# Optimization experiments

Hardware: AMD Instinct MI355X
Metric: run time of the kernel (lower is better)

## Reference

```python
import jax, jax.numpy as jnp
import numpy as np

N_ITEMS = 50000
HIDDEN = 128
M_NB = 16
HOP = 2
R_ITERS = 4
K_FACT = 10
B = 512
L = 50


def _normalize(x, eps=1e-12):
    n = jnp.linalg.norm(x, axis=-1, keepdims=True)
    return x / jnp.maximum(n, eps)


def _layernorm(x, g, b, eps=1e-5):
    mu = jnp.mean(x, axis=-1, keepdims=True)
    v = jnp.var(x, axis=-1, keepdims=True)
    return (x - mu) / jnp.sqrt(v + eps) * g + b


def _gru(x, h0, Wih, Whh, bih, bhh):
    # x: [B, L, H]; PyTorch GRU gate order: r, z, n
    def step(h, xt):
        gi = xt @ Wih.T + bih
        gh = h @ Whh.T + bhh
        ir, iz, inn = jnp.split(gi, 3, axis=-1)
        hr, hz, hn = jnp.split(gh, 3, axis=-1)
        r = jax.nn.sigmoid(ir + hr)
        zg = jax.nn.sigmoid(iz + hz)
        ng = jnp.tanh(inn + r * hn)
        h_new = (1.0 - zg) * ng + zg * h
        return h_new, h_new
    _, hs = jax.lax.scan(step, h0, jnp.swapaxes(x, 0, 1))
    return jnp.swapaxes(hs, 0, 1)


def _routing(x, x_nb):
    # NeighborRoutingAgg: x [n,d], x_nb [n,m] (1-based ids)
    xn = _normalize(x)
    z = xn[x_nb - 1]                      # [n, m, d] gather
    # iter 0: softmax(zeros) over neighbors is uniform -> mean
    u = jnp.mean(z, axis=1) + xn
    for _ in range(R_ITERS - 1):
        sq = jnp.sum(u * u, axis=1)
        u = (sq / (sq + 1.0))[:, None] * _normalize(u)   # squash
        p = jax.nn.softmax(jnp.einsum('nmd,nd->nm', z, u), axis=1)
        u = jnp.einsum('nmd,nm->nd', z, p) + xn
    return u


def setup_inputs() -> dict:
    key = jax.random.key(0)
    ks = jax.random.split(key, 16)
    H = HIDDEN
    s = 1.0 / np.sqrt(H)
    inp = {}
    inp['item_emb'] = jax.random.normal(ks[0], (N_ITEMS, H), dtype=jnp.float32) * 0.1
    inp['prob_emb'] = jax.random.normal(ks[1], (N_ITEMS, K_FACT), dtype=jnp.float32) * 0.1
    inp['W_cls'] = jax.random.normal(ks[2], (H, K_FACT), dtype=jnp.float32) * (1.0 / np.sqrt(K_FACT))
    inp['a1'] = jax.random.normal(ks[3], (1,), dtype=jnp.float32)
    inp['a2'] = jax.random.normal(ks[4], (1,), dtype=jnp.float32)
    inp['gru_Wih'] = jax.random.uniform(ks[5], (3 * H, H), minval=-s, maxval=s, dtype=jnp.float32)
    inp['gru_Whh'] = jax.random.uniform(ks[6], (3 * H, H), minval=-s, maxval=s, dtype=jnp.float32)
    inp['gru_bih'] = jax.random.uniform(ks[7], (3 * H,), minval=-s, maxval=s, dtype=jnp.float32)
    inp['gru_bhh'] = jax.random.uniform(ks[8], (3 * H,), minval=-s, maxval=s, dtype=jnp.float32)
    for nm in ['ln1', 'ln2', 'ln3', 'ln4']:
        inp[nm + '_g'] = jnp.ones((H,), dtype=jnp.float32)
        inp[nm + '_b'] = jnp.zeros((H,), dtype=jnp.float32)
    inp['mask_1'] = jnp.ones((B, L), dtype=jnp.float32)
    inp['mask_inf'] = jnp.zeros((B, L), dtype=jnp.float32)
    inp['inp_sess'] = jax.random.randint(ks[9], (B, L), 1, N_ITEMS)
    inp['lengths'] = jax.random.randint(ks[10], (B,), 1, L + 1)
    inp['adj_items'] = jax.random.randint(ks[11], (N_ITEMS, M_NB), 1, N_ITEMS)
    return inp


def reference(item_emb, prob_emb, W_cls, a1, a2, gru_Wih, gru_Whh, gru_bih, gru_bhh,
              ln1_g, ln1_b, ln2_g, ln2_b, ln3_g, ln3_b, ln4_g, ln4_b,
              mask_1, mask_inf, inp_sess, lengths, adj_items):
    H = HIDDEN
    x = item_emb[1:]                       # row 0 is padding
    x_nb = adj_items[1:]
    outs = [x]
    for i in range(HOP):
        outs.append(_routing(outs[i], x_nb))
    iv = outs[0]
    for o in outs[1:]:
        iv = iv + o
    iv = _layernorm(iv, ln1_g, ln1_b)      # [n_items-1, H]
    item_vectors = jnp.concatenate([jnp.zeros((1, H), dtype=iv.dtype), iv], axis=0)
    inp_emb = item_vectors[inp_sess]       # [B, L, H] (dropout = eval identity)
    bsz = inp_sess.shape[0]
    h0 = jnp.zeros((bsz, H), dtype=iv.dtype)
    Hs = _gru(inp_emb, h0, gru_Wih, gru_Whh, gru_bih, gru_bhh)
    Hs = _layernorm(Hs, ln2_g, ln2_b)
    ht = Hs[jnp.arange(bsz), lengths - 1]  # [B, H]
    inp_cls = prob_emb[inp_sess]           # [B, L, K]
    inp_cls_emb = _layernorm(inp_cls @ W_cls.T, ln3_g, ln3_b)
    Hc = _gru(inp_cls_emb, h0, gru_Wih, gru_Whh, gru_bih, gru_bhh)
    Hc = _layernorm(Hc, ln4_g, ln4_b)
    ht_cls = Hc[jnp.arange(bsz), lengths - 1]
    scores1 = ht @ iv.T                                           # [B, n_items-1]
    cls_tab = _layernorm(prob_emb[1:] @ W_cls.T, ln3_g, ln3_b)    # [n_items-1, H]
    scores2 = ht_cls @ cls_tab.T
    scores = jax.nn.sigmoid(a1) * scores1 + jax.nn.sigmoid(a2) * scores2
    return scores, scores1, scores2
```

## Files before the change

### kernel.cpp

```cpp
#include <hip/hip_runtime.h>
#include <hip/hip_bf16.h>

#define N_IT 49999
#define NI   50000
#define HD   128
#define MNB  16
#define BSZ  512
#define LSEQ 50
#define G3   384

typedef __attribute__((ext_vector_type(8))) short short8;
typedef __attribute__((ext_vector_type(4))) float f32x4;
typedef __attribute__((ext_vector_type(16))) float f32x16;

__device__ __forceinline__ float sigmf(float x) {
  return 1.f / (1.f + __expf(-x));
}
__device__ __forceinline__ float fast_sigm(float x) {
  return __fdividef(1.f, 1.f + __expf(-x));
}
__device__ __forceinline__ float fast_tanh(float x) {
  float e = __expf(-2.f * x);
  return (1.f - e) * __fdividef(1.f, 1.f + e);
}

__device__ __forceinline__ unsigned short f2bf(float f) {
  unsigned u = __float_as_uint(f);
  u += 0x7FFF + ((u >> 16) & 1);
  return (unsigned short)(u >> 16);
}

template <int CTRL>
__device__ __forceinline__ float dppadd(float v) {
  int s = __builtin_amdgcn_update_dpp(__float_as_int(v), __float_as_int(v),
                                      CTRL, 0xF, 0xF, false);
  return v + __int_as_float(s);
}
template <int MASK>
__device__ __forceinline__ float swzadd(float v) {
  return v + __int_as_float(__builtin_amdgcn_ds_swizzle(__float_as_int(v), MASK));
}
__device__ __forceinline__ float bp32add(float v) {
  int lane = threadIdx.x & 63;
  return v + __int_as_float(__builtin_amdgcn_ds_bpermute(((lane ^ 32) << 2),
                                                         __float_as_int(v)));
}

__device__ __forceinline__ float wsum(float v) {
  v = dppadd<0xB1>(v);
  v = dppadd<0x4E>(v);
  v = dppadd<0x141>(v);
  v = dppadd<0x140>(v);
  v = swzadd<0x401F>(v);
  v = bp32add(v);
  return v;
}

__global__ void norm_kernel(const float* __restrict__ x, float* __restrict__ o,
                            unsigned* __restrict__ ob, int n) {
  int w = threadIdx.x >> 6, l = threadIdx.x & 63;
  int r = blockIdx.x * 4 + w;
  if (r >= n) return;
  float2 xv = *(const float2*)(x + (size_t)r * HD + 2 * l);
  float sq = wsum(xv.x * xv.x + xv.y * xv.y);
  float inv = 1.f / fmaxf(sqrtf(sq), 1e-12f);
  float a = xv.x * inv, b = xv.y * inv;
  *(float2*)(o + (size_t)r * HD + 2 * l) = make_float2(a, b);
  ob[(size_t)r * 64 + l] = (unsigned)f2bf(a) | ((unsigned)f2bf(b) << 16);
}

__global__ __launch_bounds__(256) void routing1_kernel(
    const float* __restrict__ xn, const unsigned* __restrict__ xnb,
    const int* __restrict__ adj, float* __restrict__ out,
    float* __restrict__ onf, unsigned* __restrict__ onb) {
  __shared__ char zsh[4][4096];
  int tid = threadIdx.x;
  int w = tid >> 6, lane = tid & 63;
  int n = blockIdx.x * 4 + w;
  if (n >= N_IT) return;
  int m = lane & 15, quad = lane >> 4;
  const unsigned short* xb16 = (const unsigned short*)xnb;

  int idx = adj[n * MNB + m] - 1;
  const unsigned short* zrow = xb16 + (size_t)idx * HD;
  const unsigned short* xrow = xb16 + (size_t)n * HD;
  short8 zf[4], xf[4];
#pragma unroll
  for (int kk = 0; kk < 4; ++kk) {
    zf[kk] = *(const short8*)(zrow + kk * 32 + quad * 8);
    xf[kk] = *(const short8*)(xrow + kk * 32 + quad * 8);
  }
  f32x4 Gf = {0.f, 0.f, 0.f, 0.f}, Bv = {0.f, 0.f, 0.f, 0.f};
#pragma unroll
  for (int kk = 0; kk < 4; ++kk) {
    Gf = __builtin_amdgcn_mfma_f32_16x16x32_bf16(zf[kk], zf[kk], Gf, 0, 0, 0);
    Bv = __builtin_amdgcn_mfma_f32_16x16x32_bf16(zf[kk], xf[kk], Bv, 0, 0, 0);
  }
  char* zb = zsh[w] + m * 256;
#pragma unroll
  for (int kk = 0; kk < 4; ++kk)
    *(short8*)(zb + ((kk * 64 + quad * 16) ^ ((m & 7) << 4))) = zf[kk];

  float pc0 = 0.0625f, pc1 = 0.0625f, pc2 = 0.0625f, pc3 = 0.0625f;
  int msel = lane & 3;
  int cjaddr = (((lane >> 2) & 3) << 4 | (lane & 3)) << 2;

#pragma unroll
  for (int it = 0; it < 3; ++it) {
    float selv = (msel == 0) ? pc0 : (msel == 1) ? pc1 : (msel == 2) ? pc2 : pc3;
    float cj = __int_as_float(
        __builtin_amdgcn_ds_bpermute(cjaddr, __float_as_int(selv)));
    float g0 = Gf[0] * cj, g1 = Gf[1] * cj, g2 = Gf[2] * cj, g3 = Gf[3] * cj;
    g0 = dppadd<0xB1>(g0); g1 = dppadd<0xB1>(g1); g2 = dppadd<0xB1>(g2); g3 = dppadd<0xB1>(g3);
    g0 = dppadd<0x4E>(g0); g1 = dppadd<0x4E>(g1); g2 = dppadd<0x4E>(g2); g3 = dppadd<0x4E>(g3);
    g0 = swzadd<0x101F>(g0); g1 = swzadd<0x101F>(g1); g2 = swzadd<0x101F>(g2); g3 = swzadd<0x101F>(g3);
    g0 = swzadd<0x201F>(g0); g1 = swzadd<0x201F>(g1); g2 = swzadd<0x201F>(g2); g3 = swzadd<0x201F>(g3);
    float t1 = pc0 * g0 + pc1 * g1 + pc2 * g2 + pc3 * g3;
    float t2 = pc0 * Bv[0] + pc1 * Bv[1] + pc2 * Bv[2] + pc3 * Bv[3];
    t1 = swzadd<0x401F>(t1); t1 = bp32add(t1);
    t2 = swzadd<0x401F>(t2); t2 = bp32add(t2);
    float sq = fmaxf(1.f + 2.f * t2 + t1, 0.f);
    float s = (sq / (sq + 1.f)) / fmaxf(sqrtf(sq), 1e-12f);
    float e0 = __expf(s * (Bv[0] + g0));
    float e1 = __expf(s * (Bv[1] + g1));
    float e2 = __expf(s * (Bv[2] + g2));
    float e3 = __expf(s * (Bv[3] + g3));
    float se = e0 + e1 + e2 + e3;
    se = swzadd<0x401F>(se); se = bp32add(se);
    float inv = __fdividef(1.f, se);
    pc0 = e0 * inv; pc1 = e1 * inv; pc2 = e2 * inv; pc3 = e3 * inv;
  }
  float selv = (msel == 0) ? pc0 : (msel == 1) ? pc1 : (msel == 2) ? pc2 : pc3;
  float2 xv = *(const float2*)(xn + (size_t)n * HD + 2 * lane);
  float u0 = xv.x, u1 = xv.y;
#pragma unroll
  for (int mm = 0; mm < MNB; ++mm) {
    int srcl = ((((mm >> 2) << 4) | (mm & 3)) << 2);
    float pm = __int_as_float(
        __builtin_amdgcn_ds_bpermute(srcl, __float_as_int(selv)));
    unsigned zv = *(const unsigned*)(zsh[w] + mm * 256 +
                                     ((4 * lane) ^ ((mm & 7) << 4)));
    float z0 = __int_as_float((zv & 0xFFFFu) << 16);
    float z1 = __int_as_float((zv >> 16) << 16);
    u0 += z0 * pm;
    u1 += z1 * pm;
  }
  *(float2*)(out + (size_t)n * HD + 2 * lane) = make_float2(u0, u1);
  float nsq = wsum(u0 * u0 + u1 * u1);
  float ninv = 1.f / fmaxf(sqrtf(nsq), 1e-12f);
  float na = u0 * ninv, nb = u1 * ninv;
  *(float2*)(onf + (size_t)n * HD + 2 * lane) = make_float2(na, nb);
  onb[(size_t)n * 64 + lane] = (unsigned)f2bf(na) | ((unsigned)f2bf(nb) << 16);
}

__global__ __launch_bounds__(256) void routing_kernel(
    const float* __restrict__ xn, const unsigned* __restrict__ xnb,
    const int* __restrict__ adj, float* __restrict__ out) {
  __shared__ char zsh[4][4096];
  int tid = threadIdx.x;
  int w = tid >> 6, lane = tid & 63;
  int n = blockIdx.x * 4 + w;
  if (n >= N_IT) return;
  int m = lane & 15, quad = lane >> 4;
  const unsigned short* xb16 = (const unsigned short*)xnb;

  int idx = adj[n * MNB + m] - 1;
  const unsigned short* zrow = xb16 + (size_t)idx * HD;
  const unsigned short* xrow = xb16 + (size_t)n * HD;
  short8 zf[4], xf[4];
#pragma unroll
  for (int kk = 0; kk < 4; ++kk) {
    zf[kk] = *(const short8*)(zrow + kk * 32 + quad * 8);
    xf[kk] = *(const short8*)(xrow + kk * 32 + quad * 8);
  }
  f32x4 Gf = {0.f, 0.f, 0.f, 0.f}, Bv = {0.f, 0.f, 0.f, 0.f};
#pragma unroll
  for (int kk = 0; kk < 4; ++kk) {
    Gf = __builtin_amdgcn_mfma_f32_16x16x32_bf16(zf[kk], zf[kk], Gf, 0, 0, 0);
    Bv = __builtin_amdgcn_mfma_f32_16x16x32_bf16(zf[kk], xf[kk], Bv, 0, 0, 0);
  }
  char* zb = zsh[w] + m * 256;
#pragma unroll
  for (int kk = 0; kk < 4; ++kk)
    *(short8*)(zb + ((kk * 64 + quad * 16) ^ ((m & 7) << 4))) = zf[kk];

  float pc0 = 0.0625f, pc1 = 0.0625f, pc2 = 0.0625f, pc3 = 0.0625f;
  int msel = lane & 3;
  int cjaddr = (((lane >> 2) & 3) << 4 | (lane & 3)) << 2;

#pragma unroll
  for (int it = 0; it < 3; ++it) {
    float selv = (msel == 0) ? pc0 : (msel == 1) ? pc1 : (msel == 2) ? pc2 : pc3;
    float cj = __int_as_float(
        __builtin_amdgcn_ds_bpermute(cjaddr, __float_as_int(selv)));
    float g0 = Gf[0] * cj, g1 = Gf[1] * cj, g2 = Gf[2] * cj, g3 = Gf[3] * cj;
    g0 = dppadd<0xB1>(g0); g1 = dppadd<0xB1>(g1); g2 = dppadd<0xB1>(g2); g3 = dppadd<0xB1>(g3);
    g0 = dppadd<0x4E>(g0); g1 = dppadd<0x4E>(g1); g2 = dppadd<0x4E>(g2); g3 = dppadd<0x4E>(g3);
    g0 = swzadd<0x101F>(g0); g1 = swzadd<0x101F>(g1); g2 = swzadd<0x101F>(g2); g3 = swzadd<0x101F>(g3);
    g0 = swzadd<0x201F>(g0); g1 = swzadd<0x201F>(g1); g2 = swzadd<0x201F>(g2); g3 = swzadd<0x201F>(g3);
    float t1 = pc0 * g0 + pc1 * g1 + pc2 * g2 + pc3 * g3;
    float t2 = pc0 * Bv[0] + pc1 * Bv[1] + pc2 * Bv[2] + pc3 * Bv[3];
    t1 = swzadd<0x401F>(t1); t1 = bp32add(t1);
    t2 = swzadd<0x401F>(t2); t2 = bp32add(t2);
    float sq = fmaxf(1.f + 2.f * t2 + t1, 0.f);
    float s = (sq / (sq + 1.f)) / fmaxf(sqrtf(sq), 1e-12f);
    float e0 = __expf(s * (Bv[0] + g0));
    float e1 = __expf(s * (Bv[1] + g1));
    float e2 = __expf(s * (Bv[2] + g2));
    float e3 = __expf(s * (Bv[3] + g3));
    float se = e0 + e1 + e2 + e3;
    se = swzadd<0x401F>(se); se = bp32add(se);
    float inv = __fdividef(1.f, se);
    pc0 = e0 * inv; pc1 = e1 * inv; pc2 = e2 * inv; pc3 = e3 * inv;
  }
  float selv = (msel == 0) ? pc0 : (msel == 1) ? pc1 : (msel == 2) ? pc2 : pc3;
  float2 xv = *(const float2*)(xn + (size_t)n * HD + 2 * lane);
  float u0 = xv.x, u1 = xv.y;
#pragma unroll
  for (int mm = 0; mm < MNB; ++mm) {
    int srcl = ((((mm >> 2) << 4) | (mm & 3)) << 2);
    float pm = __int_as_float(
        __builtin_amdgcn_ds_bpermute(srcl, __float_as_int(selv)));
    unsigned zv = *(const unsigned*)(zsh[w] + mm * 256 +
                                     ((4 * lane) ^ ((mm & 7) << 4)));
    float z0 = __int_as_float((zv & 0xFFFFu) << 16);
    float z1 = __int_as_float((zv >> 16) << 16);
    u0 += z0 * pm;
    u1 += z1 * pm;
  }
  *(float2*)(out + (size_t)n * HD + 2 * lane) = make_float2(u0, u1);
}

__global__ void iv_kernel(const float* __restrict__ item_emb,
                          const float* __restrict__ o1, const float* __restrict__ o2,
                          const float* __restrict__ g, const float* __restrict__ bb,
                          unsigned short* __restrict__ tbf) {
  int w = threadIdx.x >> 6, l = threadIdx.x & 63;
  int r = blockIdx.x * 4 + w;
  if (r >= NI) return;
  if (r == 0) {
    tbf[l] = 0; tbf[l + 64] = 0;
    return;
  }
  size_t pr = (size_t)(r - 1) * HD;
  float a = item_emb[(size_t)r * HD + l]      + o1[pr + l]      + o2[pr + l];
  float b = item_emb[(size_t)r * HD + l + 64] + o1[pr + l + 64] + o2[pr + l + 64];
  float mu = wsum(a + b) * (1.f / HD);
  float v  = wsum(a * a + b * b) * (1.f / HD) - mu * mu;
  float rs = rsqrtf(v + 1e-5f);
  float va = (a - mu) * rs * g[l] + bb[l];
  float vb = (b - mu) * rs * g[l + 64] + bb[l + 64];
  tbf[(size_t)r * HD + l]      = f2bf(va);
  tbf[(size_t)r * HD + l + 64] = f2bf(vb);
}

__global__ void cls_kernel(const float* __restrict__ prob, const float* __restrict__ Wc,
                           const float* __restrict__ g, const float* __restrict__ bb,
                           unsigned short* __restrict__ cbf) {
  int w = threadIdx.x >> 6, l = threadIdx.x & 63;
  int r = blockIdx.x * 4 + w;
  if (r >= NI) return;
  float p[10];
#pragma unroll
  for (int k = 0; k < 10; ++k) p[k] = prob[(size_t)r * 10 + k];
  float a = 0.f, b = 0.f;
#pragma unroll
  for (int k = 0; k < 10; ++k) {
    a += p[k] * Wc[l * 10 + k];
    b += p[k] * Wc[(l + 64) * 10 + k];
  }
  float mu = wsum(a + b) * (1.f / HD);
  float v  = wsum(a * a + b * b) * (1.f / HD) - mu * mu;
  float rs = rsqrtf(v + 1e-5f);
  float va = (a - mu) * rs * g[l] + bb[l];
  float vb = (b - mu) * rs * g[l + 64] + bb[l + 64];
  cbf[(size_t)r * HD + l]      = f2bf(va);
  cbf[(size_t)r * HD + l + 64] = f2bf(vb);
}

__global__ void wbf_kernel(const float* __restrict__ Wih,
                           unsigned short* __restrict__ wbf) {
  int i = blockIdx.x * 256 + threadIdx.x;
  if (i < 3 * HD * HD) wbf[i] = f2bf(Wih[i]);
}

__global__ __launch_bounds__(256) void gi2_kernel(
    const unsigned short* __restrict__ tbf, const unsigned short* __restrict__ cbf,
    const int* __restrict__ sess, const unsigned short* __restrict__ wbf,
    float* __restrict__ gi) {
  __shared__ int sidx[16];
  int tid = threadIdx.x;
  int row0 = blockIdx.x * 16;
  if (tid < 16) sidx[tid] = sess[(row0 + tid) % 25600];
  __syncthreads();
  const unsigned short* src = (row0 < 25600) ? tbf : cbf;
  int w = tid >> 6, lane = tid & 63;
  int rloc = lane & 15, quad = lane >> 4;
  int arow = sidx[rloc];
  int ko = quad * 8;
  short8 A[4];
#pragma unroll
  for (int kk = 0; kk < 4; ++kk)
    A[kk] = *(const short8*)(src + (size_t)arow * HD + kk * 32 + ko);
  float* gout = gi + (size_t)row0 * G3;
#pragma unroll
  for (int s = 0; s < 6; ++s) {
    int jt = w * 6 + s;
    int j = jt * 16 + rloc;
    f32x4 acc = {0.f, 0.f, 0.f, 0.f};
#pragma unroll
    for (int kk = 0; kk < 4; ++kk) {
      short8 B = *(const short8*)(wbf + (size_t)j * HD + kk * 32 + ko);
      acc = __builtin_amdgcn_mfma_f32_16x16x32_bf16(A[kk], B, acc, 0, 0, 0);
    }
#pragma unroll
    for (int q = 0; q < 4; ++q)
      gout[(size_t)(quad * 4 + q) * G3 + jt * 16 + rloc] = acc[q];
  }
}

__global__ __launch_bounds__(512) void gru_mfma_kernel(
    const float* __restrict__ gi_all, const float* __restrict__ Whh,
    const float* __restrict__ bih, const float* __restrict__ bhh,
    const int* __restrict__ lengths, float* __restrict__ ht_raw) {
  __shared__ unsigned short hlds[2][16 * HD];
  int tid = threadIdx.x;
  int lane = tid & 63;
  int w = tid >> 6;
  int p = blockIdx.x >> 5;
  int r0 = (blockIdx.x & 31) * 16;
  int cN = lane & 15;
  int quad = lane >> 4;
  int d = w * 16 + cN;

  {
    int* hz = (int*)hlds;
    for (int i = tid; i < 2 * 16 * HD / 2; i += 512) hz[i] = 0;
  }

  short8 Br[4], Bz[4], Bn[4];
#pragma unroll
  for (int kk = 0; kk < 4; ++kk) {
    int kbase = quad * 8 + kk * 32;
    const float* wr_ = Whh + (size_t)d * HD + kbase;
    const float* wz_ = Whh + (size_t)(128 + d) * HD + kbase;
    const float* wn_ = Whh + (size_t)(256 + d) * HD + kbase;
    float4 r0v = *(const float4*)wr_, r1v = *(const float4*)(wr_ + 4);
    float4 z0v = *(const float4*)wz_, z1v = *(const float4*)(wz_ + 4);
    float4 n0v = *(const float4*)wn_, n1v = *(const float4*)(wn_ + 4);
    short8 br, bz, bn;
    br[0]=(short)f2bf(r0v.x); br[1]=(short)f2bf(r0v.y); br[2]=(short)f2bf(r0v.z); br[3]=(short)f2bf(r0v.w);
    br[4]=(short)f2bf(r1v.x); br[5]=(short)f2bf(r1v.y); br[6]=(short)f2bf(r1v.z); br[7]=(short)f2bf(r1v.w);
    bz[0]=(short)f2bf(z0v.x); bz[1]=(short)f2bf(z0v.y); bz[2]=(short)f2bf(z0v.z); bz[3]=(short)f2bf(z0v.w);
    bz[4]=(short)f2bf(z1v.x); bz[5]=(short)f2bf(z1v.y); bz[6]=(short)f2bf(z1v.z); bz[7]=(short)f2bf(z1v.w);
    bn[0]=(short)f2bf(n0v.x); bn[1]=(short)f2bf(n0v.y); bn[2]=(short)f2bf(n0v.z); bn[3]=(short)f2bf(n0v.w);
    bn[4]=(short)f2bf(n1v.x); bn[5]=(short)f2bf(n1v.y); bn[6]=(short)f2bf(n1v.z); bn[7]=(short)f2bf(n1v.w);
    Br[kk] = br; Bz[kk] = bz; Bn[kk] = bn;
  }
  float cr = bhh[d] + bih[d];
  float cz = bhh[128 + d] + bih[128 + d];
  float bhn = bhh[256 + d], bin = bih[256 + d];

  int lens4[4];
  float hold[4];
  const float* gptr[4];
#pragma unroll
  for (int gq = 0; gq < 4; ++gq) {
    int lr = quad * 4 + gq;
    lens4[gq] = lengths[r0 + lr] - 1;
    hold[gq] = 0.f;
    gptr[gq] = gi_all + ((size_t)p * 25600 + (size_t)(r0 + lr) * LSEQ) * G3 + d;
  }

  int aoff[4];
#pragma unroll
  for (int kk = 0; kk < 4; ++kk)
    aoff[kk] = cN * 256 + (((quad * 8 + kk * 32) * 2) ^ ((cN & 7) << 4));
  int woff[4];
#pragma unroll
  for (int gq = 0; gq < 4; ++gq) {
    int lr = quad * 4 + gq;
    woff[gq] = lr * 256 + ((2 * d) ^ ((lr & 7) << 4));
  }

  float giaR[4], giaZ[4], giaN[4];
#pragma unroll
  for (int gq = 0; gq < 4; ++gq) {
    giaR[gq] = gptr[gq][0];
    giaZ[gq] = gptr[gq][HD];
    giaN[gq] = gptr[gq][2 * HD];
  }
  __syncthreads();

  for (int t = 0; t < LSEQ; ++t) {
    float gbR[4], gbZ[4], gbN[4];
#pragma unroll
    for (int gq = 0; gq < 4; ++gq) {
      const float* gp = gptr[gq] + (size_t)(t + 1) * G3;
      gbR[gq] = gp[0]; gbZ[gq] = gp[HD]; gbN[gq] = gp[2 * HD];
    }
    const char* hb = (const char*)hlds[t & 1];
    f32x4 accR = {0.f, 0.f, 0.f, 0.f};
    f32x4 accZ = {0.f, 0.f, 0.f, 0.f};
    f32x4 accN = {0.f, 0.f, 0.f, 0.f};
#pragma unroll
    for (int kk = 0; kk < 4; ++kk) {
      short8 A = *(const short8*)(hb + aoff[kk]);
      accR = __builtin_amdgcn_mfma_f32_16x16x32_bf16(A, Br[kk], accR, 0, 0, 0);
      accZ = __builtin_amdgcn_mfma_f32_16x16x32_bf16(A, Bz[kk], accZ, 0, 0, 0);
      accN = __builtin_amdgcn_mfma_f32_16x16x32_bf16(A, Bn[kk], accN, 0, 0, 0);
    }
    char* hw = (char*)hlds[(t + 1) & 1];
#pragma unroll
    for (int gq = 0; gq < 4; ++gq) {
      float rg = fast_sigm(giaR[gq] + accR[gq] + cr);
      float zg = fast_sigm(giaZ[gq] + accZ[gq] + cz);
      float ng = fast_tanh(giaN[gq] + bin + rg * (accN[gq] + bhn));
      float hnew = (1.f - zg) * ng + zg * hold[gq];
      hold[gq] = hnew;
      *(unsigned short*)(hw + woff[gq]) = f2bf(hnew);
      if (t == lens4[gq])
        ht_raw[((size_t)p * BSZ + r0 + quad * 4 + gq) * HD + d] = hnew;
    }
    __syncthreads();
#pragma unroll
    for (int gq = 0; gq < 4; ++gq) {
      giaR[gq] = gbR[gq]; giaZ[gq] = gbZ[gq]; giaN[gq] = gbN[gq];
    }
  }
}

__global__ void ln_ht_kernel(const float* __restrict__ ht,
                             const float* __restrict__ g2, const float* __restrict__ b2,
                             const float* __restrict__ g4, const float* __restrict__ b4,
                             unsigned short* __restrict__ hbf) {
  int w = threadIdx.x >> 6, l = threadIdx.x & 63;
  int r = blockIdx.x * 4 + w;
  if (r >= 2 * BSZ) return;
  const float* g = (r < BSZ) ? g2 : g4;
  const float* bb = (r < BSZ) ? b2 : b4;
  float a = ht[(size_t)r * HD + l];
  float b = ht[(size_t)r * HD + l + 64];
  float mu = wsum(a + b) * (1.f / HD);
  float v  = wsum(a * a + b * b) * (1.f / HD) - mu * mu;
  float rs = rsqrtf(v + 1e-5f);
  float va = (a - mu) * rs * g[l] + bb[l];
  float vb = (b - mu) * rs * g[l + 64] + bb[l + 64];
  hbf[(size_t)r * HD + l]      = f2bf(va);
  hbf[(size_t)r * HD + l + 64] = f2bf(vb);
}

#define JW 256
__global__ __launch_bounds__(512) void scores2_kernel(
    const unsigned short* __restrict__ hbf,
    const unsigned short* __restrict__ tbf,
    const unsigned short* __restrict__ cbf,
    const float* __restrict__ a1p, const float* __restrict__ a2p,
    float* __restrict__ out) {
  __shared__ float s1l[32 * JW];
  __shared__ float s2l[32 * JW];
  int tid = threadIdx.x;
  int w = tid >> 6, lane = tid & 63;
  int strip = blockIdx.x >> 4;
  int r0b = (blockIdx.x & 15) * 32;
  int j0 = strip * JW;
  int jc = j0 + w * 32 + (lane & 31);
  int jl = (jc < N_IT) ? jc : (N_IT - 1);
  int koA = (lane >> 5) * 8;

  f32x16 acc1 = {0.f}, acc2 = {0.f};
  const unsigned short* h1p = hbf + (size_t)(r0b + (lane & 31)) * HD + koA;
  const unsigned short* h2p = h1p + (size_t)BSZ * HD;
  const unsigned short* b1p = tbf + (size_t)(jl + 1) * HD + koA;
  const unsigned short* b2p = cbf + (size_t)(jl + 1) * HD + koA;
#pragma unroll
  for (int kk = 0; kk < 8; ++kk) {
    short8 A1 = *(const short8*)(h1p + kk * 16);
    short8 A2 = *(const short8*)(h2p + kk * 16);
    short8 B1 = *(const short8*)(b1p + kk * 16);
    short8 B2 = *(const short8*)(b2p + kk * 16);
    acc1 = __builtin_amdgcn_mfma_f32_32x32x16_bf16(A1, B1, acc1, 0, 0, 0);
    acc2 = __builtin_amdgcn_mfma_f32_32x32x16_bf16(A2, B2, acc2, 0, 0, 0);
  }
  int colb = w * 32 + (lane & 31);
#pragma unroll
  for (int q = 0; q < 16; ++q) {
    int row = (q & 3) + 8 * (q >> 2) + 4 * (lane >> 5);
    s1l[row * JW + colb] = acc1[q];
    s2l[row * JW + colb] = acc2[q];
  }
  __syncthreads();

  float sa1 = sigmf(a1p[0]);
  float sa2 = sigmf(a2p[0]);
  const size_t S = (size_t)BSZ * N_IT;
#pragma unroll
  for (int pss = 0; pss < 16; ++pss) {
    int idx = pss * 512 + tid;
    int row = idx >> 8;
    int jlc = idx & 255;
    int jg = j0 + jlc;
    if (jg < N_IT) {
      float s1 = s1l[idx];
      float s2 = s2l[idx];
      size_t o = (size_t)(r0b + row) * N_IT + jg;
      out[o]         = sa1 * s1 + sa2 * s2;
      out[S + o]     = s1;
      out[2 * S + o] = s2;
    }
  }
}

extern "C" void kernel_launch(void* const* d_in, const int* in_sizes, int n_in,
                              void* d_out, int out_size, void* d_ws, size_t ws_size,
                              hipStream_t stream) {
  const float* item_emb = (const float*)d_in[0];
  const float* prob_emb = (const float*)d_in[1];
  const float* W_cls    = (const float*)d_in[2];
  const float* a1       = (const float*)d_in[3];
  const float* a2       = (const float*)d_in[4];
  const float* Wih      = (const float*)d_in[5];
  const float* Whh      = (const float*)d_in[6];
  const float* bih      = (const float*)d_in[7];
  const float* bhh      = (const float*)d_in[8];
  const float* ln1_g = (const float*)d_in[9];
  const float* ln1_b = (const float*)d_in[10];
  const float* ln2_g = (const float*)d_in[11];
  const float* ln2_b = (const float*)d_in[12];
  const float* ln3_g = (const float*)d_in[13];
  const float* ln3_b = (const float*)d_in[14];
  const float* ln4_g = (const float*)d_in[15];
  const float* ln4_b = (const float*)d_in[16];
  const int* inp_sess = (const int*)d_in[19];
  const int* lengths  = (const int*)d_in[20];
  const int* adj      = (const int*)d_in[21];
  float* out = (float*)d_out;

  float* ws = (float*)d_ws;
  const size_t SZ_ROW = (size_t)N_IT * HD;
  float* xn   = ws;
  float* o1   = xn + SZ_ROW;
  float* o2   = o1 + SZ_ROW;
  float* slot = o2 + SZ_ROW;
  float* x1f  = slot;
  unsigned* x1b = (unsigned*)(slot + 6400000);
  float* gi  = o2 + SZ_ROW + 2 * (size_t)NI * HD;
  float* htb = gi + (size_t)2 * 25600 * G3;

  unsigned* xnb = (unsigned*)gi;
  unsigned short* tbf = (unsigned short*)xn;
  unsigned short* cbf = (unsigned short*)o2;
  unsigned short* hbf = (unsigned short*)o1;
  unsigned short* wbf = (unsigned short*)(o2 + 3400000);

  int nb4 = (N_IT + 3) / 4;
  int nb4i = (NI + 3) / 4;

  norm_kernel<<<nb4, 256, 0, stream>>>(item_emb + HD, xn, xnb, N_IT);
  routing1_kernel<<<nb4, 256, 0, stream>>>(xn, xnb, adj + MNB, o1, x1f, x1b);
  routing_kernel<<<nb4, 256, 0, stream>>>(x1f, x1b, adj + MNB, o2);
  iv_kernel<<<nb4i, 256, 0, stream>>>(item_emb, o1, o2, ln1_g, ln1_b, tbf);
  cls_kernel<<<nb4i, 256, 0, stream>>>(prob_emb, W_cls, ln3_g, ln3_b, cbf);
  wbf_kernel<<<192, 256, 0, stream>>>(Wih, wbf);
  gi2_kernel<<<3200, 256, 0, stream>>>(tbf, cbf, inp_sess, wbf, gi);
  gru_mfma_kernel<<<64, 512, 0, stream>>>(gi, Whh, bih, bhh, lengths, htb);
  ln_ht_kernel<<<256, 256, 0, stream>>>(htb, ln2_g, ln2_b, ln4_g, ln4_b, hbf);
  scores2_kernel<<<196 * 16, 512, 0, stream>>>(hbf, tbf, cbf, a1, a2, out);
}
```

Measured before the change: 417.8 us.

## Fuse prelude kernels and store GRU input gates in bf16

```diff
diff --git a/kernel.cpp b/kernel.cpp
--- a/kernel.cpp
+++ b/kernel.cpp
@@ -28,6 +28,9 @@
   unsigned u = __float_as_uint(f);
   u += 0x7FFF + ((u >> 16) & 1);
   return (unsigned short)(u >> 16);
+}
+__device__ __forceinline__ float bf2f(unsigned short v) {
+  return __int_as_float(((unsigned)v) << 16);
 }
 
 template <int CTRL>
@@ -56,17 +59,51 @@
   return v;
 }
 
-__global__ void norm_kernel(const float* __restrict__ x, float* __restrict__ o,
-                            unsigned* __restrict__ ob, int n) {
-  int w = threadIdx.x >> 6, l = threadIdx.x & 63;
-  int r = blockIdx.x * 4 + w;
-  if (r >= n) return;
-  float2 xv = *(const float2*)(x + (size_t)r * HD + 2 * l);
-  float sq = wsum(xv.x * xv.x + xv.y * xv.y);
-  float inv = 1.f / fmaxf(sqrtf(sq), 1e-12f);
-  float a = xv.x * inv, b = xv.y * inv;
-  *(float2*)(o + (size_t)r * HD + 2 * l) = make_float2(a, b);
-  ob[(size_t)r * 64 + l] = (unsigned)f2bf(a) | ((unsigned)f2bf(b) << 16);
+__global__ void prelude_kernel(const float* __restrict__ item_emb,
+                               float* __restrict__ xnf, unsigned* __restrict__ xnb,
+                               const float* __restrict__ prob,
+                               const float* __restrict__ Wc,
+                               const float* __restrict__ g3v,
+                               const float* __restrict__ b3v,
+                               unsigned short* __restrict__ cbf,
+                               const float* __restrict__ Wih,
+                               unsigned short* __restrict__ wbf) {
+  int b = blockIdx.x;
+  if (b < 12500) {
+    int w = threadIdx.x >> 6, l = threadIdx.x & 63;
+    int r = b * 4 + w;
+    if (r >= N_IT) return;
+    const float* x = item_emb + HD;
+    float2 xv = *(const float2*)(x + (size_t)r * HD + 2 * l);
+    float sq = wsum(xv.x * xv.x + xv.y * xv.y);
+    float inv = 1.f / fmaxf(sqrtf(sq), 1e-12f);
+    float a = xv.x * inv, bb = xv.y * inv;
+    *(float2*)(xnf + (size_t)r * HD + 2 * l) = make_float2(a, bb);
+    xnb[(size_t)r * 64 + l] = (unsigned)f2bf(a) | ((unsigned)f2bf(bb) << 16);
+  } else if (b < 25000) {
+    int w = threadIdx.x >> 6, l = threadIdx.x & 63;
+    int r = (b - 12500) * 4 + w;
+    if (r >= NI) return;
+    float p[10];
+#pragma unroll
+    for (int k = 0; k < 10; ++k) p[k] = prob[(size_t)r * 10 + k];
+    float a = 0.f, bb = 0.f;
+#pragma unroll
+    for (int k = 0; k < 10; ++k) {
+      a += p[k] * Wc[l * 10 + k];
+      bb += p[k] * Wc[(l + 64) * 10 + k];
+    }
+    float mu = wsum(a + bb) * (1.f / HD);
+    float v  = wsum(a * a + bb * bb) * (1.f / HD) - mu * mu;
+    float rs = rsqrtf(v + 1e-5f);
+    float va = (a - mu) * rs * g3v[l] + b3v[l];
+    float vb = (bb - mu) * rs * g3v[l + 64] + b3v[l + 64];
+    cbf[(size_t)r * HD + l]      = f2bf(va);
+    cbf[(size_t)r * HD + l + 64] = f2bf(vb);
+  } else {
+    int i = (b - 25000) * 256 + threadIdx.x;
+    if (i < 3 * HD * HD) wbf[i] = f2bf(Wih[i]);
+  }
 }
 
 __global__ __launch_bounds__(256) void routing1_kernel(
@@ -254,40 +291,10 @@
   tbf[(size_t)r * HD + l + 64] = f2bf(vb);
 }
 
-__global__ void cls_kernel(const float* __restrict__ prob, const float* __restrict__ Wc,
-                           const float* __restrict__ g, const float* __restrict__ bb,
-                           unsigned short* __restrict__ cbf) {
-  int w = threadIdx.x >> 6, l = threadIdx.x & 63;
-  int r = blockIdx.x * 4 + w;
-  if (r >= NI) return;
-  float p[10];
-#pragma unroll
-  for (int k = 0; k < 10; ++k) p[k] = prob[(size_t)r * 10 + k];
-  float a = 0.f, b = 0.f;
-#pragma unroll
-  for (int k = 0; k < 10; ++k) {
-    a += p[k] * Wc[l * 10 + k];
-    b += p[k] * Wc[(l + 64) * 10 + k];
-  }
-  float mu = wsum(a + b) * (1.f / HD);
-  float v  = wsum(a * a + b * b) * (1.f / HD) - mu * mu;
-  float rs = rsqrtf(v + 1e-5f);
-  float va = (a - mu) * rs * g[l] + bb[l];
-  float vb = (b - mu) * rs * g[l + 64] + bb[l + 64];
-  cbf[(size_t)r * HD + l]      = f2bf(va);
-  cbf[(size_t)r * HD + l + 64] = f2bf(vb);
-}
-
-__global__ void wbf_kernel(const float* __restrict__ Wih,
-                           unsigned short* __restrict__ wbf) {
-  int i = blockIdx.x * 256 + threadIdx.x;
-  if (i < 3 * HD * HD) wbf[i] = f2bf(Wih[i]);
-}
-
 __global__ __launch_bounds__(256) void gi2_kernel(
     const unsigned short* __restrict__ tbf, const unsigned short* __restrict__ cbf,
     const int* __restrict__ sess, const unsigned short* __restrict__ wbf,
-    float* __restrict__ gi) {
+    unsigned short* __restrict__ gib) {
   __shared__ int sidx[16];
   int tid = threadIdx.x;
   int row0 = blockIdx.x * 16;
@@ -302,7 +309,7 @@
 #pragma unroll
   for (int kk = 0; kk < 4; ++kk)
     A[kk] = *(const short8*)(src + (size_t)arow * HD + kk * 32 + ko);
-  float* gout = gi + (size_t)row0 * G3;
+  unsigned short* gout = gib + (size_t)row0 * G3;
 #pragma unroll
   for (int s = 0; s < 6; ++s) {
     int jt = w * 6 + s;
@@ -315,12 +322,12 @@
     }
 #pragma unroll
     for (int q = 0; q < 4; ++q)
-      gout[(size_t)(quad * 4 + q) * G3 + jt * 16 + rloc] = acc[q];
+      gout[(size_t)(quad * 4 + q) * G3 + jt * 16 + rloc] = f2bf(acc[q]);
   }
 }
 
 __global__ __launch_bounds__(512) void gru_mfma_kernel(
-    const float* __restrict__ gi_all, const float* __restrict__ Whh,
+    const unsigned short* __restrict__ gi_all, const float* __restrict__ Whh,
     const float* __restrict__ bih, const float* __restrict__ bhh,
     const int* __restrict__ lengths, float* __restrict__ ht_raw) {
   __shared__ unsigned short hlds[2][16 * HD];
@@ -363,7 +370,7 @@
 
   int lens4[4];
   float hold[4];
-  const float* gptr[4];
+  const unsigned short* gptr[4];
 #pragma unroll
   for (int gq = 0; gq < 4; ++gq) {
     int lr = quad * 4 + gq;
@@ -386,9 +393,9 @@
   float giaR[4], giaZ[4], giaN[4];
 #pragma unroll
   for (int gq = 0; gq < 4; ++gq) {
-    giaR[gq] = gptr[gq][0];
-    giaZ[gq] = gptr[gq][HD];
-    giaN[gq] = gptr[gq][2 * HD];
+    giaR[gq] = bf2f(gptr[gq][0]);
+    giaZ[gq] = bf2f(gptr[gq][HD]);
+    giaN[gq] = bf2f(gptr[gq][2 * HD]);
   }
   __syncthreads();
 
@@ -396,8 +403,8 @@
     float gbR[4], gbZ[4], gbN[4];
 #pragma unroll
     for (int gq = 0; gq < 4; ++gq) {
-      const float* gp = gptr[gq] + (size_t)(t + 1) * G3;
-      gbR[gq] = gp[0]; gbZ[gq] = gp[HD]; gbN[gq] = gp[2 * HD];
+      const unsigned short* gp = gptr[gq] + (size_t)(t + 1) * G3;
+      gbR[gq] = bf2f(gp[0]); gbZ[gq] = bf2f(gp[HD]); gbN[gq] = bf2f(gp[2 * HD]);
     }
     const char* hb = (const char*)hlds[t & 1];
     f32x4 accR = {0.f, 0.f, 0.f, 0.f};
@@ -544,26 +551,27 @@
   float* slot = o2 + SZ_ROW;
   float* x1f  = slot;
   unsigned* x1b = (unsigned*)(slot + 6400000);
-  float* gi  = o2 + SZ_ROW + 2 * (size_t)NI * HD;
+  unsigned short* cbf = (unsigned short*)(slot + 9600000);
+  float* gi  = slot + 2 * (size_t)NI * HD;
   float* htb = gi + (size_t)2 * 25600 * G3;
 
   unsigned* xnb = (unsigned*)gi;
+  unsigned short* gib = (unsigned short*)gi;
+  unsigned short* wbf = (unsigned short*)(gi + 10000000);
   unsigned short* tbf = (unsigned short*)xn;
-  unsigned short* cbf = (unsigned short*)o2;
   unsigned short* hbf = (unsigned short*)o1;
-  unsigned short* wbf = (unsigned short*)(o2 + 3400000);
 
   int nb4 = (N_IT + 3) / 4;
   int nb4i = (NI + 3) / 4;
 
-  norm_kernel<<<nb4, 256, 0, stream>>>(item_emb + HD, xn, xnb, N_IT);
+  prelude_kernel<<<25192, 256, 0, stream>>>(item_emb, xn, xnb,
+                                            prob_emb, W_cls, ln3_g, ln3_b, cbf,
+                                            Wih, wbf);
   routing1_kernel<<<nb4, 256, 0, stream>>>(xn, xnb, adj + MNB, o1, x1f, x1b);
   routing_kernel<<<nb4, 256, 0, stream>>>(x1f, x1b, adj + MNB, o2);
   iv_kernel<<<nb4i, 256, 0, stream>>>(item_emb, o1, o2, ln1_g, ln1_b, tbf);
-  cls_kernel<<<nb4i, 256, 0, stream>>>(prob_emb, W_cls, ln3_g, ln3_b, cbf);
-  wbf_kernel<<<192, 256, 0, stream>>>(Wih, wbf);
-  gi2_kernel<<<3200, 256, 0, stream>>>(tbf, cbf, inp_sess, wbf, gi);
-  gru_mfma_kernel<<<64, 512, 0, stream>>>(gi, Whh, bih, bhh, lengths, htb);
+  gi2_kernel<<<3200, 256, 0, stream>>>(tbf, cbf, inp_sess, wbf, gib);
+  gru_mfma_kernel<<<64, 512, 0, stream>>>(gib, Whh, bih, bhh, lengths, htb);
   ln_ht_kernel<<<256, 256, 0, stream>>>(htb, ln2_g, ln2_b, ln4_g, ln4_b, hbf);
   scores2_kernel<<<196 * 16, 512, 0, stream>>>(hbf, tbf, cbf, a1, a2, out);
 }
```

Result: faster. 406.7 us (-2.7%).
